# Optimization experiments

Measured on AMD Instinct MI355X. Metric: run time of the kernel, lower is better.

The kernel has to match this reference:

```python
import jax, jax.numpy as jnp
import numpy as np

N_E = 8192
E_DIM = 64
EPS = 1e-12  # torch F.normalize eps


def l2_normalize(x):
    n = jnp.linalg.norm(x, axis=-1, keepdims=True)
    return x / jnp.maximum(n, EPS)


def setup_inputs() -> dict:
    key = jax.random.key(0)
    k1, k2 = jax.random.split(key)
    z = jax.random.normal(k1, (8, E_DIM, 64, 64), dtype=jnp.float32)  # [B, C, H, W]
    # init: uniform(-1/n_e, 1/n_e) then L2-normalized (l2_norm=True)
    emb = jax.random.uniform(k2, (N_E, E_DIM), dtype=jnp.float32,
                             minval=-1.0 / N_E, maxval=1.0 / N_E)
    emb = l2_normalize(emb)
    return {"z": z, "embedding": emb}


def reference(z, embedding):
    # b c h w -> b h w c
    zt = jnp.transpose(z, (0, 2, 3, 1))
    zn = l2_normalize(zt)                      # l2_norm=True path
    z_flat = zn.reshape(-1, zn.shape[-1])      # [B*H*W, e_dim]
    e = l2_normalize(embedding)                # [n_e, e_dim]

    # squared L2 distances: ||z||^2 + ||e||^2 - 2 z e^T
    d = (jnp.sum(z_flat ** 2, axis=1, keepdims=True)
         + jnp.sum(e ** 2, axis=1)
         - 2.0 * jnp.einsum('bd,nd->bn', z_flat, e))  # [B*H*W, n_e]

    min_encoding_indices = jnp.argmin(d, axis=1)       # [B*H*W]
    z_q = e[min_encoding_indices].reshape(zn.shape)    # gather codebook

    # straight-through estimator (eval mode: commit_loss is None)
    z_q = zn + jax.lax.stop_gradient(z_q - zn)
    z_q = jnp.transpose(z_q, (0, 3, 1, 2))             # b h w c -> b c h w
    return z_q, min_encoding_indices
```

## Files before the change

kernel.cpp:

```cpp
#include <hip/hip_runtime.h>


#define NPIX 32768
#define NE   8192
#define EDIM 64
#define HW   4096
#define NSTAGE 128
#define KSPLIT 8
#define CPS  (NE / KSPLIT)
#define NSTG (CPS / NSTAGE)
#define MARGIN1 6.0e-4f
#define NSET 2

typedef _Float16 f16x8 __attribute__((ext_vector_type(8)));
typedef float f32x4  __attribute__((ext_vector_type(4)));

__device__ __forceinline__ short f2h_bits(float x) {
    _Float16 h = (_Float16)x;
    short s; __builtin_memcpy(&s, &h, 2); return s;
}
__device__ __forceinline__ unsigned int order_u32(float f) {
    unsigned int s = __float_as_uint(f);
    return (s & 0x80000000u) ? ~s : (s | 0x80000000u);
}
__device__ __forceinline__ void gload_lds16(const void* g, void* l) {
    __builtin_amdgcn_global_load_lds(
        (const __attribute__((address_space(1))) void*)g,
        (__attribute__((address_space(3))) void*)l, 16, 0, 0);
}

__global__ __launch_bounds__(256) void k_prep(const float* __restrict__ emb,
                                              const float* __restrict__ z,
                                              float* __restrict__ e_norm,
                                              float* __restrict__ se_half,
                                              short* __restrict__ esw,
                                              float* __restrict__ zn,
                                              unsigned* __restrict__ counter) {
    if (blockIdx.x == 0 && threadIdx.x == 0) counter[0] = 0u;
    if (blockIdx.x < NE / 4) {
        const int wave = threadIdx.x >> 6;
        const int lane = threadIdx.x & 63;
        const int n = blockIdx.x * 4 + wave;
        float v = emb[n * EDIM + lane];
        float ss = v * v;
        #pragma unroll
        for (int off = 32; off; off >>= 1) ss += __shfl_xor(ss, off, 64);
        const float inv = 1.0f / fmaxf(sqrtf(ss), 1e-12f);
        const float en = v * inv;
        e_norm[n * EDIM + lane] = en;
        const int grp = n >> 6, cs = n & 63;
        const int sub = cs >> 4, colb = cs & 15;
        const int o = lane >> 3, j = lane & 7;
        const int slot = ((o & 3) * 16 + colb) * 8 + j;
        esw[grp * 4096 + (sub * 2 + (o >> 2)) * 512 + slot] = f2h_bits(en);
        float s2 = en * en;
        #pragma unroll
        for (int off = 32; off; off >>= 1) s2 += __shfl_xor(s2, off, 64);
        if (lane == 0) se_half[n] = 0.5f * s2;
    } else {
        const int p = (blockIdx.x - NE / 4) * 256 + threadIdx.x;
        const int b = p >> 12, hw = p & (HW - 1);
        const float* zp = z + b * (EDIM * HW) + hw;
        float v[EDIM];
        #pragma unroll
        for (int c = 0; c < EDIM; ++c) v[c] = zp[c * HW];
        float ss = 0.0f;
        #pragma unroll
        for (int c = 0; c < EDIM; ++c) ss = fmaf(v[c], v[c], ss);
        const float inv = 1.0f / fmaxf(sqrtf(ss), 1e-12f);
        #pragma unroll
        for (int c4 = 0; c4 < 16; ++c4) {
            float4 o;
            o.x = v[c4 * 4 + 0] * inv;
            o.y = v[c4 * 4 + 1] * inv;
            o.z = v[c4 * 4 + 2] * inv;
            o.w = v[c4 * 4 + 3] * inv;
            *(float4*)(zn + p * EDIM + c4 * 4) = o;
        }
    }
}

__global__ __launch_bounds__(256, 1) void k_mfma(const float* __restrict__ zn,
                                                 const short* __restrict__ esw,
                                                 float2* __restrict__ pv,
                                                 unsigned* __restrict__ pi)
{
    __shared__ __align__(16) short es[2][NSTAGE * EDIM];

    const int tid  = threadIdx.x;
    const int wave = tid >> 6, lane = tid & 63;
    const int quad = lane >> 4, col = lane & 15;
    const int p0   = blockIdx.x * 128 + wave * 32;
    const int g    = blockIdx.y;
    const int kbase = g * CPS;

    f16x8 ah[NSET][2];
    #pragma unroll
    for (int s = 0; s < NSET; ++s) {
        const float* zr = zn + (p0 + s * 16 + col) * EDIM;
        #pragma unroll
        for (int kc = 0; kc < 2; ++kc) {
            float f[8];
            *(float4*)(f + 0) = *(const float4*)(zr + kc * 32 + quad * 8 + 0);
            *(float4*)(f + 4) = *(const float4*)(zr + kc * 32 + quad * 8 + 4);
            #pragma unroll
            for (int i = 0; i < 8; ++i) ah[s][kc][i] = (_Float16)f[i];
        }
    }

    float b1[NSET][4], b2[NSET][4];
    #pragma unroll
    for (int s = 0; s < NSET; ++s)
        #pragma unroll
        for (int r = 0; r < 4; ++r) { b1[s][r] = 0.0f; b2[s][r] = 0.0f; }

    const f32x4 cini = {2.0f, 2.0f, 2.0f, 2.0f};

    const int combo0 = wave * 4;
    const char* gsrc0 = (const char*)esw + (size_t)kbase * 128
                        + combo0 * 1024 + lane * 16;
    #pragma unroll
    for (int it = 0; it < 4; ++it)
        gload_lds16(gsrc0 + it * 1024, (char*)&es[0][0] + (combo0 + it) * 1024);

    for (int nb = 0; nb < NSTG; ++nb) {
        const int cur = nb & 1;
        __syncthreads();
        if (nb + 1 < NSTG) {
            const char* gsrc = gsrc0 + (size_t)(nb + 1) * (NSTAGE * EDIM * 2);
            #pragma unroll
            for (int it = 0; it < 4; ++it)
                gload_lds16(gsrc + it * 1024,
                            (char*)&es[cur ^ 1][0] + (combo0 + it) * 1024);
        }

        const short* esb = es[cur];
        #pragma unroll
        for (int sub = 0; sub < 8; ++sub) {
            const short* base = esb + sub * 1024;
            const f16x8 bh0 = *(const f16x8*)(base + lane * 8);
            const f16x8 bh1 = *(const f16x8*)(base + 512 + lane * 8);
            const unsigned sid = (unsigned)((nb << 3) | sub);
            #pragma unroll
            for (int s = 0; s < NSET; ++s) {
                f32x4 acc;
                acc = __builtin_amdgcn_mfma_f32_16x16x32_f16(ah[s][0], bh0, cini, 0, 0, 0);
                acc = __builtin_amdgcn_mfma_f32_16x16x32_f16(ah[s][1], bh1, acc, 0, 0, 0);
                #pragma unroll
                for (int r = 0; r < 4; ++r) {
                    const float v = __uint_as_float(
                        (__float_as_uint(acc[r]) & 0xFFFFFFC0u) | sid);
                    b2[s][r] = __builtin_amdgcn_fmed3f(v, b2[s][r], b1[s][r]);
                    b1[s][r] = fmaxf(b1[s][r], v);
                }
            }
        }
    }

    int i1[NSET][4];
    #pragma unroll
    for (int s = 0; s < NSET; ++s)
        #pragma unroll
        for (int r = 0; r < 4; ++r) {
            const unsigned id6 = __float_as_uint(b1[s][r]) & 63u;
            i1[s][r] = kbase + (int)(id6 << 4) + col;
        }

    #pragma unroll
    for (int m = 1; m <= 8; m <<= 1) {
        #pragma unroll
        for (int s = 0; s < NSET; ++s)
            #pragma unroll
            for (int r = 0; r < 4; ++r) {
                const float ob1 = __shfl_xor(b1[s][r], m, 64);
                const int   oi1 = __shfl_xor(i1[s][r], m, 64);
                const float ob2 = __shfl_xor(b2[s][r], m, 64);
                const bool take = (ob1 > b1[s][r]) || (ob1 == b1[s][r] && oi1 < i1[s][r]);
                b2[s][r] = fmaxf(fmaxf(b2[s][r], ob2), fminf(b1[s][r], ob1));
                b1[s][r] = take ? ob1 : b1[s][r];
                i1[s][r] = take ? oi1 : i1[s][r];
            }
    }
    if (col == 0) {
        #pragma unroll
        for (int s = 0; s < NSET; ++s)
            #pragma unroll
            for (int r = 0; r < 4; ++r) {
                const int p = p0 + s * 16 + quad * 4 + r;
                pv[g * NPIX + p] = make_float2(b1[s][r], b2[s][r]);
                pi[g * NPIX + p] = (unsigned)i1[s][r];
            }
    }
}

__global__ __launch_bounds__(256) void k_merge(const float2* __restrict__ pv,
                                               const unsigned* __restrict__ pi,
                                               const float* __restrict__ zn,
                                               const float* __restrict__ e_norm,
                                               const float* __restrict__ se_half,
                                               unsigned* __restrict__ idx_arr,
                                               unsigned* __restrict__ list2,
                                               unsigned* __restrict__ counter,
                                               unsigned long long* __restrict__ packed) {
    const int p = blockIdx.x * 256 + threadIdx.x;
    float2 v[KSPLIT]; unsigned ix[KSPLIT];
    #pragma unroll
    for (int gg = 0; gg < KSPLIT; ++gg) {
        v[gg] = pv[gg * NPIX + p];
        ix[gg] = pi[gg * NPIX + p];
    }
    float gb1 = v[0].x; unsigned gi1 = ix[0]; int win = 0;
    #pragma unroll
    for (int gg = 1; gg < KSPLIT; ++gg)
        if (v[gg].x > gb1) { gb1 = v[gg].x; gi1 = ix[gg]; win = gg; }
    float gb2 = -3.0e38f;
    #pragma unroll
    for (int gg = 0; gg < KSPLIT; ++gg) {
        gb2 = fmaxf(gb2, v[gg].y);
        if (gg != win) gb2 = fmaxf(gb2, v[gg].x);
    }
    const float thr = gb1 - MARGIN1;
    if (gb2 < thr) {
        idx_arr[p] = gi1;
        return;
    }
    bool esc = false;
    #pragma unroll
    for (int gg = 0; gg < KSPLIT; ++gg) esc |= (v[gg].y >= thr);
    if (esc) {
        packed[p] = ~0ull;
        idx_arr[p] = 0x80000000u | gi1;
        const unsigned pos = atomicAdd(&counter[0], 1u);
        if (pos < NPIX) list2[pos] = p;
        return;
    }
    float zr[EDIM];
    #pragma unroll
    for (int c4 = 0; c4 < 16; ++c4)
        *(float4*)(zr + c4 * 4) = *(const float4*)(zn + (size_t)p * EDIM + c4 * 4);
    float best = 3.0e38f; int bidx = 0x7FFFFFFF;
    #pragma unroll
    for (int gg = 0; gg < KSPLIT; ++gg) {
        if (v[gg].x >= thr) {
            const int c = (int)ix[gg];
            const float* er = e_norm + (size_t)c * EDIM;
            float s = 0.0f;
            #pragma unroll
            for (int k = 0; k < EDIM; ++k) s = fmaf(zr[k], er[k], s);
            const float d = se_half[c] - s;
            if (d < best || (d == best && c < bidx)) { best = d; bidx = c; }
        }
    }
    idx_arr[p] = (unsigned)bidx;
}

__global__ __launch_bounds__(256) void k_recheck(const float* __restrict__ zn,
                                                 const float* __restrict__ e_norm,
                                                 const float* __restrict__ se_half,
                                                 const unsigned* __restrict__ list2,
                                                 const unsigned* __restrict__ counter,
                                                 unsigned long long* __restrict__ packed) {
    const int lane  = threadIdx.x & 63;
    const int k     = lane >> 4;
    const int m     = lane & 15;
    const int wglob = (blockIdx.x * 256 + threadIdx.x) >> 6;
    const int nwav  = (gridDim.x * 256) >> 6;
    int cnt = (int)counter[0]; if (cnt > NPIX) cnt = NPIX;
    const int nitems = cnt * 16;
    const float4* e4 = (const float4*)e_norm;

    for (int item = wglob; item < nitems; item += nwav) {
        const int p     = (int)list2[item >> 4];
        const int chunk = item & 15;
        const float4 zv = *(const float4*)(zn + (size_t)p * EDIM + m * 4);
        float best = 3.0e38f; int bidx = 0;
        for (int t4 = 0; t4 < 32; ++t4) {
            float s[4]; int n[4];
            #pragma unroll
            for (int j = 0; j < 4; ++j) {
                n[j] = chunk * 512 + (t4 * 4 + j) * 4 + k;
                const float4 ev = e4[n[j] * 16 + m];
                s[j] = fmaf(zv.w, ev.w, fmaf(zv.z, ev.z,
                       fmaf(zv.y, ev.y, zv.x * ev.x)));
            }
            #pragma unroll
            for (int j = 0; j < 4; ++j) s[j] += __shfl_xor(s[j], 1, 64);
            #pragma unroll
            for (int j = 0; j < 4; ++j) s[j] += __shfl_xor(s[j], 2, 64);
            #pragma unroll
            for (int j = 0; j < 4; ++j) s[j] += __shfl_xor(s[j], 4, 64);
            #pragma unroll
            for (int j = 0; j < 4; ++j) s[j] += __shfl_xor(s[j], 8, 64);
            #pragma unroll
            for (int j = 0; j < 4; ++j) {
                const float d = se_half[n[j]] - s[j];
                if (d < best) { best = d; bidx = n[j]; }
            }
        }
        #pragma unroll
        for (int mm = 1; mm <= 32; mm <<= 1) {
            const float ob = __shfl_xor(best, mm, 64);
            const int   oi = __shfl_xor(bidx, mm, 64);
            if (ob < best || (ob == best && oi < bidx)) { best = ob; bidx = oi; }
        }
        if (lane == 0) {
            const unsigned long long key =
                ((unsigned long long)order_u32(best) << 32) | (unsigned)bidx;
            atomicMin(&packed[p], key);
        }
    }
}

__global__ __launch_bounds__(256) void k_finalize(const unsigned* __restrict__ idx_arr,
                                                  const unsigned long long* __restrict__ packed,
                                                  const float* __restrict__ e_norm,
                                                  float* __restrict__ out) {
    const int pl = threadIdx.x & 63;
    const int q  = threadIdx.x >> 6;
    const int p  = blockIdx.x * 64 + pl;
    const unsigned v = idx_arr[p];
    const int bidx = (v & 0x80000000u) ? (int)(packed[p] & 0xFFFFFFFFull)
                                       : (int)v;
    if (q == 0) out[NPIX * EDIM + p] = (float)bidx;
    const int b = p >> 12, hw = p & (HW - 1);
    float* op = out + b * (EDIM * HW) + hw;
    const float4* ep4 = (const float4*)(e_norm + (size_t)bidx * EDIM + q * 16);
    #pragma unroll
    for (int j = 0; j < 4; ++j) {
        const float4 e = ep4[j];
        const int c = q * 16 + j * 4;
        op[(c + 0) * HW] = e.x; op[(c + 1) * HW] = e.y;
        op[(c + 2) * HW] = e.z; op[(c + 3) * HW] = e.w;
    }
}

extern "C" void kernel_launch(void* const* d_in, const int* in_sizes, int n_in,
                              void* d_out, int out_size, void* d_ws, size_t ws_size,
                              hipStream_t stream) {
    const float* z   = (const float*)d_in[0];
    const float* emb = (const float*)d_in[1];
    float* out = (float*)d_out;

    float* e_norm  = (float*)d_ws;
    float* se_half = e_norm + NE * EDIM;
    short* esw = (short*)(se_half + NE);
    float* zn = (float*)(esw + NE * EDIM);
    unsigned* idx_arr = (unsigned*)(zn + NPIX * EDIM);
    unsigned* list2   = idx_arr + NPIX;
    unsigned* counter = list2 + NPIX;
    unsigned long long* packed = (unsigned long long*)(counter + 64);
    float2*   pv = (float2*)(packed + NPIX);
    unsigned* pi = (unsigned*)(pv + KSPLIT * NPIX);

    k_prep<<<NE / 4 + NPIX / 256, 256, 0, stream>>>(emb, z, e_norm, se_half,
                                                    esw, zn, counter);
    k_mfma<<<dim3(NPIX / 128, KSPLIT), 256, 0, stream>>>(zn, esw, pv, pi);
    k_merge<<<NPIX / 256, 256, 0, stream>>>(pv, pi, zn, e_norm, se_half,
                                            idx_arr, list2, counter, packed);
    k_recheck<<<1024, 256, 0, stream>>>(zn, e_norm, se_half, list2, counter, packed);
    k_finalize<<<NPIX / 64, 256, 0, stream>>>(idx_arr, packed, e_norm, out);
}
```

Before: 165.3 us.

## Fuse merge, recheck and finalize into one per-block post kernel

Replaces the three kernels that ran after the MFMA pass (merge, global recheck queue, finalize) with a single kernel. Each 64-pixel block merges the split partial results, keeps its own work queue of full-codebook rescans in shared memory, resolves them with shared-memory atomicMin, and writes the output. This removes two launches, the global counter and list, and the round trips through global memory. The cost is that rescans are no longer spread across the whole GPU, so blocks holding many ambiguous pixels can become stragglers. Ambiguous pixels are also now split per partition (two chunks per flagged split) rather than scanning the whole codebook.

```diff
diff --git a/kernel.cpp b/kernel.cpp
--- a/kernel.cpp
+++ b/kernel.cpp
@@ -34,9 +34,7 @@
                                               float* __restrict__ e_norm,
                                               float* __restrict__ se_half,
                                               short* __restrict__ esw,
-                                              float* __restrict__ zn,
-                                              unsigned* __restrict__ counter) {
-    if (blockIdx.x == 0 && threadIdx.x == 0) counter[0] = 0u;
+                                              float* __restrict__ zn) {
     if (blockIdx.x < NE / 4) {
         const int wave = threadIdx.x >> 6;
         const int lane = threadIdx.x & 63;
@@ -193,85 +191,89 @@
     }
 }
 
-__global__ __launch_bounds__(256) void k_merge(const float2* __restrict__ pv,
-                                               const unsigned* __restrict__ pi,
-                                               const float* __restrict__ zn,
-                                               const float* __restrict__ e_norm,
-                                               const float* __restrict__ se_half,
-                                               unsigned* __restrict__ idx_arr,
-                                               unsigned* __restrict__ list2,
-                                               unsigned* __restrict__ counter,
-                                               unsigned long long* __restrict__ packed) {
-    const int p = blockIdx.x * 256 + threadIdx.x;
-    float2 v[KSPLIT]; unsigned ix[KSPLIT];
-    #pragma unroll
-    for (int gg = 0; gg < KSPLIT; ++gg) {
-        v[gg] = pv[gg * NPIX + p];
-        ix[gg] = pi[gg * NPIX + p];
-    }
-    float gb1 = v[0].x; unsigned gi1 = ix[0]; int win = 0;
-    #pragma unroll
-    for (int gg = 1; gg < KSPLIT; ++gg)
-        if (v[gg].x > gb1) { gb1 = v[gg].x; gi1 = ix[gg]; win = gg; }
-    float gb2 = -3.0e38f;
-    #pragma unroll
-    for (int gg = 0; gg < KSPLIT; ++gg) {
-        gb2 = fmaxf(gb2, v[gg].y);
-        if (gg != win) gb2 = fmaxf(gb2, v[gg].x);
-    }
-    const float thr = gb1 - MARGIN1;
-    if (gb2 < thr) {
-        idx_arr[p] = gi1;
-        return;
-    }
-    bool esc = false;
-    #pragma unroll
-    for (int gg = 0; gg < KSPLIT; ++gg) esc |= (v[gg].y >= thr);
-    if (esc) {
-        packed[p] = ~0ull;
-        idx_arr[p] = 0x80000000u | gi1;
-        const unsigned pos = atomicAdd(&counter[0], 1u);
-        if (pos < NPIX) list2[pos] = p;
-        return;
-    }
-    float zr[EDIM];
-    #pragma unroll
-    for (int c4 = 0; c4 < 16; ++c4)
-        *(float4*)(zr + c4 * 4) = *(const float4*)(zn + (size_t)p * EDIM + c4 * 4);
-    float best = 3.0e38f; int bidx = 0x7FFFFFFF;
-    #pragma unroll
-    for (int gg = 0; gg < KSPLIT; ++gg) {
-        if (v[gg].x >= thr) {
-            const int c = (int)ix[gg];
-            const float* er = e_norm + (size_t)c * EDIM;
-            float s = 0.0f;
-            #pragma unroll
-            for (int k = 0; k < EDIM; ++k) s = fmaf(zr[k], er[k], s);
-            const float d = se_half[c] - s;
-            if (d < best || (d == best && c < bidx)) { best = d; bidx = c; }
-        }
-    }
-    idx_arr[p] = (unsigned)bidx;
-}
-
-__global__ __launch_bounds__(256) void k_recheck(const float* __restrict__ zn,
-                                                 const float* __restrict__ e_norm,
-                                                 const float* __restrict__ se_half,
-                                                 const unsigned* __restrict__ list2,
-                                                 const unsigned* __restrict__ counter,
-                                                 unsigned long long* __restrict__ packed) {
-    const int lane  = threadIdx.x & 63;
-    const int k     = lane >> 4;
-    const int m     = lane & 15;
-    const int wglob = (blockIdx.x * 256 + threadIdx.x) >> 6;
-    const int nwav  = (gridDim.x * 256) >> 6;
-    int cnt = (int)counter[0]; if (cnt > NPIX) cnt = NPIX;
-    const int nitems = cnt * 16;
+__global__ __launch_bounds__(256) void k_post(const float2* __restrict__ pv,
+                                              const unsigned* __restrict__ pi,
+                                              const float* __restrict__ zn,
+                                              const float* __restrict__ e_norm,
+                                              const float* __restrict__ se_half,
+                                              float* __restrict__ out) {
+    __shared__ unsigned s_q[1024];
+    __shared__ unsigned long long s_key[64];
+    __shared__ int s_idx[64];
+    __shared__ int s_qcnt;
+
+    const int tid  = threadIdx.x;
+    const int wave = tid >> 6, lane = tid & 63;
+    const int p0   = blockIdx.x * 64;
+
+    if (tid == 0) s_qcnt = 0;
+    __syncthreads();
+
+    if (wave == 0) {
+        const int p = p0 + lane;
+        float2 v[KSPLIT]; unsigned ix[KSPLIT];
+        #pragma unroll
+        for (int gg = 0; gg < KSPLIT; ++gg) {
+            v[gg] = pv[gg * NPIX + p];
+            ix[gg] = pi[gg * NPIX + p];
+        }
+        float gb1 = v[0].x; unsigned gi1 = ix[0]; int win = 0;
+        #pragma unroll
+        for (int gg = 1; gg < KSPLIT; ++gg)
+            if (v[gg].x > gb1) { gb1 = v[gg].x; gi1 = ix[gg]; win = gg; }
+        float gb2 = -3.0e38f;
+        #pragma unroll
+        for (int gg = 0; gg < KSPLIT; ++gg) {
+            gb2 = fmaxf(gb2, v[gg].y);
+            if (gg != win) gb2 = fmaxf(gb2, v[gg].x);
+        }
+        const float thr = gb1 - MARGIN1;
+        int idx; unsigned long long key = ~0ull; bool esc = false;
+        if (gb2 < thr) {
+            idx = (int)gi1;
+        } else {
+            float zr[EDIM];
+            #pragma unroll
+            for (int c4 = 0; c4 < 16; ++c4)
+                *(float4*)(zr + c4 * 4) =
+                    *(const float4*)(zn + (size_t)p * EDIM + c4 * 4);
+            float best = 3.0e38f; int bidx = 0x7FFFFFFF;
+            #pragma unroll
+            for (int gg = 0; gg < KSPLIT; ++gg) {
+                if (v[gg].x >= thr) {
+                    const int c = (int)ix[gg];
+                    const float* er = e_norm + (size_t)c * EDIM;
+                    float s = 0.0f;
+                    #pragma unroll
+                    for (int k = 0; k < EDIM; ++k) s = fmaf(zr[k], er[k], s);
+                    const float d = se_half[c] - s;
+                    if (d < best || (d == best && c < bidx)) { best = d; bidx = c; }
+                }
+            }
+            idx = bidx;
+            key = ((unsigned long long)order_u32(best) << 32) | (unsigned)bidx;
+            #pragma unroll
+            for (int gg = 0; gg < KSPLIT; ++gg) {
+                if (v[gg].y >= thr) {
+                    esc = true;
+                    const int base = atomicAdd(&s_qcnt, 2);
+                    s_q[base]     = (unsigned)lane | ((unsigned)(gg * 2)     << 6);
+                    s_q[base + 1] = (unsigned)lane | ((unsigned)(gg * 2 + 1) << 6);
+                }
+            }
+        }
+        s_key[lane] = key;
+        s_idx[lane] = esc ? -1 : idx;
+    }
+    __syncthreads();
+
+    const int qn = s_qcnt;
+    const int k = lane >> 4, m = lane & 15;
     const float4* e4 = (const float4*)e_norm;
-
-    for (int item = wglob; item < nitems; item += nwav) {
-        const int p     = (int)list2[item >> 4];
-        const int chunk = item & 15;
+    for (int e = wave; e < qn; e += 4) {
+        const unsigned ent = s_q[e];
+        const int pl = (int)(ent & 63u), chunk = (int)(ent >> 6);
+        const int p = p0 + pl;
         const float4 zv = *(const float4*)(zn + (size_t)p * EDIM + m * 4);
         float best = 3.0e38f; int bidx = 0;
         for (int t4 = 0; t4 < 32; ++t4) {
@@ -304,33 +306,29 @@
             if (ob < best || (ob == best && oi < bidx)) { best = ob; bidx = oi; }
         }
         if (lane == 0) {
-            const unsigned long long key =
+            const unsigned long long kk =
                 ((unsigned long long)order_u32(best) << 32) | (unsigned)bidx;
-            atomicMin(&packed[p], key);
-        }
-    }
-}
-
-__global__ __launch_bounds__(256) void k_finalize(const unsigned* __restrict__ idx_arr,
-                                                  const unsigned long long* __restrict__ packed,
-                                                  const float* __restrict__ e_norm,
-                                                  float* __restrict__ out) {
-    const int pl = threadIdx.x & 63;
-    const int q  = threadIdx.x >> 6;
-    const int p  = blockIdx.x * 64 + pl;
-    const unsigned v = idx_arr[p];
-    const int bidx = (v & 0x80000000u) ? (int)(packed[p] & 0xFFFFFFFFull)
-                                       : (int)v;
+            atomicMin(&s_key[pl], kk);
+        }
+    }
+    __syncthreads();
+    if (wave == 0 && s_idx[lane] < 0)
+        s_idx[lane] = (int)(s_key[lane] & 0xFFFFFFFFull);
+    __syncthreads();
+
+    const int p = p0 + lane;
+    const int bidx = s_idx[lane];
+    const int q = wave;
     if (q == 0) out[NPIX * EDIM + p] = (float)bidx;
     const int b = p >> 12, hw = p & (HW - 1);
     float* op = out + b * (EDIM * HW) + hw;
     const float4* ep4 = (const float4*)(e_norm + (size_t)bidx * EDIM + q * 16);
     #pragma unroll
     for (int j = 0; j < 4; ++j) {
-        const float4 e = ep4[j];
+        const float4 ev = ep4[j];
         const int c = q * 16 + j * 4;
-        op[(c + 0) * HW] = e.x; op[(c + 1) * HW] = e.y;
-        op[(c + 2) * HW] = e.z; op[(c + 3) * HW] = e.w;
+        op[(c + 0) * HW] = ev.x; op[(c + 1) * HW] = ev.y;
+        op[(c + 2) * HW] = ev.z; op[(c + 3) * HW] = ev.w;
     }
 }
 
@@ -345,18 +343,11 @@
     float* se_half = e_norm + NE * EDIM;
     short* esw = (short*)(se_half + NE);
     float* zn = (float*)(esw + NE * EDIM);
-    unsigned* idx_arr = (unsigned*)(zn + NPIX * EDIM);
-    unsigned* list2   = idx_arr + NPIX;
-    unsigned* counter = list2 + NPIX;
-    unsigned long long* packed = (unsigned long long*)(counter + 64);
-    float2*   pv = (float2*)(packed + NPIX);
+    float2*   pv = (float2*)(zn + NPIX * EDIM);
     unsigned* pi = (unsigned*)(pv + KSPLIT * NPIX);
 
     k_prep<<<NE / 4 + NPIX / 256, 256, 0, stream>>>(emb, z, e_norm, se_half,
-                                                    esw, zn, counter);
+                                                    esw, zn);
     k_mfma<<<dim3(NPIX / 128, KSPLIT), 256, 0, stream>>>(zn, esw, pv, pi);
-    k_merge<<<NPIX / 256, 256, 0, stream>>>(pv, pi, zn, e_norm, se_half,
-                                            idx_arr, list2, counter, packed);
-    k_recheck<<<1024, 256, 0, stream>>>(zn, e_norm, se_half, list2, counter, packed);
-    k_finalize<<<NPIX / 64, 256, 0, stream>>>(idx_arr, packed, e_norm, out);
-}
+    k_post<<<NPIX / 64, 256, 0, stream>>>(pv, pi, zn, e_norm, se_half, out);
+}
```

Result: slower. 175.4 us (+6.1%).

## Fuse finalize into merge/recheck and rescan only flagged codebook splits

Applied to the files above, without the earlier changes.

The merge kernel now writes the gathered codebook row and index straight to the output for resolved pixels, which removes the separate finalize kernel and its idx/packed buffers. Ambiguous pixels are queued with a bitmask of the splits whose second-best value was close, together with the exact best key found so far. The recheck kernel gives each pixel one wavefront, scans only the flagged 1024-entry splits instead of all 8192 entries, and writes the output itself. This removes a launch and most of the recheck work, but moves the strided output writes into merge and loads a single wavefront with a serial per-pixel loop.

```diff
diff --git a/kernel.cpp b/kernel.cpp
--- a/kernel.cpp
+++ b/kernel.cpp
@@ -193,16 +193,16 @@
     }
 }
 
-__global__ __launch_bounds__(256) void k_merge(const float2* __restrict__ pv,
+__global__ __launch_bounds__(128) void k_merge(const float2* __restrict__ pv,
                                                const unsigned* __restrict__ pi,
                                                const float* __restrict__ zn,
                                                const float* __restrict__ e_norm,
                                                const float* __restrict__ se_half,
-                                               unsigned* __restrict__ idx_arr,
-                                               unsigned* __restrict__ list2,
+                                               unsigned* __restrict__ list,
+                                               unsigned long long* __restrict__ lkey,
                                                unsigned* __restrict__ counter,
-                                               unsigned long long* __restrict__ packed) {
-    const int p = blockIdx.x * 256 + threadIdx.x;
+                                               float* __restrict__ out) {
+    const int p = blockIdx.x * 128 + threadIdx.x;
     float2 v[KSPLIT]; unsigned ix[KSPLIT];
     #pragma unroll
     for (int gg = 0; gg < KSPLIT; ++gg) {
@@ -220,117 +220,117 @@
         if (gg != win) gb2 = fmaxf(gb2, v[gg].x);
     }
     const float thr = gb1 - MARGIN1;
+    int bidx;
     if (gb2 < thr) {
-        idx_arr[p] = gi1;
-        return;
-    }
-    bool esc = false;
-    #pragma unroll
-    for (int gg = 0; gg < KSPLIT; ++gg) esc |= (v[gg].y >= thr);
-    if (esc) {
-        packed[p] = ~0ull;
-        idx_arr[p] = 0x80000000u | gi1;
-        const unsigned pos = atomicAdd(&counter[0], 1u);
-        if (pos < NPIX) list2[pos] = p;
-        return;
-    }
-    float zr[EDIM];
-    #pragma unroll
-    for (int c4 = 0; c4 < 16; ++c4)
-        *(float4*)(zr + c4 * 4) = *(const float4*)(zn + (size_t)p * EDIM + c4 * 4);
-    float best = 3.0e38f; int bidx = 0x7FFFFFFF;
-    #pragma unroll
-    for (int gg = 0; gg < KSPLIT; ++gg) {
-        if (v[gg].x >= thr) {
-            const int c = (int)ix[gg];
-            const float* er = e_norm + (size_t)c * EDIM;
-            float s = 0.0f;
-            #pragma unroll
-            for (int k = 0; k < EDIM; ++k) s = fmaf(zr[k], er[k], s);
-            const float d = se_half[c] - s;
-            if (d < best || (d == best && c < bidx)) { best = d; bidx = c; }
-        }
-    }
-    idx_arr[p] = (unsigned)bidx;
+        bidx = (int)gi1;
+    } else {
+        float zr[EDIM];
+        #pragma unroll
+        for (int c4 = 0; c4 < 16; ++c4)
+            *(float4*)(zr + c4 * 4) =
+                *(const float4*)(zn + (size_t)p * EDIM + c4 * 4);
+        float best = 3.0e38f; bidx = 0x7FFFFFFF;
+        #pragma unroll
+        for (int gg = 0; gg < KSPLIT; ++gg) {
+            if (v[gg].x >= thr) {
+                const int c = (int)ix[gg];
+                const float* er = e_norm + (size_t)c * EDIM;
+                float s = 0.0f;
+                #pragma unroll
+                for (int k = 0; k < EDIM; ++k) s = fmaf(zr[k], er[k], s);
+                const float d = se_half[c] - s;
+                if (d < best || (d == best && c < bidx)) { best = d; bidx = c; }
+            }
+        }
+        unsigned mask = 0;
+        #pragma unroll
+        for (int gg = 0; gg < KSPLIT; ++gg)
+            if (v[gg].y >= thr) mask |= (1u << gg);
+        if (mask) {
+            const unsigned pos = atomicAdd(&counter[0], 1u);
+            list[pos] = (unsigned)p | (mask << 16);
+            lkey[pos] = ((unsigned long long)order_u32(best) << 32) | (unsigned)bidx;
+            return;
+        }
+    }
+    out[NPIX * EDIM + p] = (float)bidx;
+    const int b = p >> 12, hw = p & (HW - 1);
+    float* op = out + b * (EDIM * HW) + hw;
+    const float4* ep4 = (const float4*)(e_norm + (size_t)bidx * EDIM);
+    #pragma unroll
+    for (int j = 0; j < 16; ++j) {
+        const float4 e = ep4[j];
+        const int c = j * 4;
+        op[(c + 0) * HW] = e.x; op[(c + 1) * HW] = e.y;
+        op[(c + 2) * HW] = e.z; op[(c + 3) * HW] = e.w;
+    }
 }
 
 __global__ __launch_bounds__(256) void k_recheck(const float* __restrict__ zn,
                                                  const float* __restrict__ e_norm,
                                                  const float* __restrict__ se_half,
-                                                 const unsigned* __restrict__ list2,
+                                                 const unsigned* __restrict__ list,
+                                                 const unsigned long long* __restrict__ lkey,
                                                  const unsigned* __restrict__ counter,
-                                                 unsigned long long* __restrict__ packed) {
+                                                 float* __restrict__ out) {
     const int lane  = threadIdx.x & 63;
     const int k     = lane >> 4;
     const int m     = lane & 15;
     const int wglob = (blockIdx.x * 256 + threadIdx.x) >> 6;
     const int nwav  = (gridDim.x * 256) >> 6;
     int cnt = (int)counter[0]; if (cnt > NPIX) cnt = NPIX;
-    const int nitems = cnt * 16;
     const float4* e4 = (const float4*)e_norm;
 
-    for (int item = wglob; item < nitems; item += nwav) {
-        const int p     = (int)list2[item >> 4];
-        const int chunk = item & 15;
+    for (int item = wglob; item < cnt; item += nwav) {
+        const unsigned e = list[item];
+        const int p = (int)(e & 0xFFFFu);
+        const unsigned mask = e >> 16;
+        unsigned long long key = lkey[item];
         const float4 zv = *(const float4*)(zn + (size_t)p * EDIM + m * 4);
-        float best = 3.0e38f; int bidx = 0;
-        for (int t4 = 0; t4 < 32; ++t4) {
-            float s[4]; int n[4];
-            #pragma unroll
-            for (int j = 0; j < 4; ++j) {
-                n[j] = chunk * 512 + (t4 * 4 + j) * 4 + k;
-                const float4 ev = e4[n[j] * 16 + m];
-                s[j] = fmaf(zv.w, ev.w, fmaf(zv.z, ev.z,
-                       fmaf(zv.y, ev.y, zv.x * ev.x)));
-            }
-            #pragma unroll
-            for (int j = 0; j < 4; ++j) s[j] += __shfl_xor(s[j], 1, 64);
-            #pragma unroll
-            for (int j = 0; j < 4; ++j) s[j] += __shfl_xor(s[j], 2, 64);
-            #pragma unroll
-            for (int j = 0; j < 4; ++j) s[j] += __shfl_xor(s[j], 4, 64);
-            #pragma unroll
-            for (int j = 0; j < 4; ++j) s[j] += __shfl_xor(s[j], 8, 64);
-            #pragma unroll
-            for (int j = 0; j < 4; ++j) {
-                const float d = se_half[n[j]] - s[j];
-                if (d < best) { best = d; bidx = n[j]; }
-            }
-        }
-        #pragma unroll
-        for (int mm = 1; mm <= 32; mm <<= 1) {
-            const float ob = __shfl_xor(best, mm, 64);
-            const int   oi = __shfl_xor(bidx, mm, 64);
-            if (ob < best || (ob == best && oi < bidx)) { best = ob; bidx = oi; }
-        }
-        if (lane == 0) {
-            const unsigned long long key =
-                ((unsigned long long)order_u32(best) << 32) | (unsigned)bidx;
-            atomicMin(&packed[p], key);
-        }
-    }
-}
-
-__global__ __launch_bounds__(256) void k_finalize(const unsigned* __restrict__ idx_arr,
-                                                  const unsigned long long* __restrict__ packed,
-                                                  const float* __restrict__ e_norm,
-                                                  float* __restrict__ out) {
-    const int pl = threadIdx.x & 63;
-    const int q  = threadIdx.x >> 6;
-    const int p  = blockIdx.x * 64 + pl;
-    const unsigned v = idx_arr[p];
-    const int bidx = (v & 0x80000000u) ? (int)(packed[p] & 0xFFFFFFFFull)
-                                       : (int)v;
-    if (q == 0) out[NPIX * EDIM + p] = (float)bidx;
-    const int b = p >> 12, hw = p & (HW - 1);
-    float* op = out + b * (EDIM * HW) + hw;
-    const float4* ep4 = (const float4*)(e_norm + (size_t)bidx * EDIM + q * 16);
-    #pragma unroll
-    for (int j = 0; j < 4; ++j) {
-        const float4 e = ep4[j];
-        const int c = q * 16 + j * 4;
-        op[(c + 0) * HW] = e.x; op[(c + 1) * HW] = e.y;
-        op[(c + 2) * HW] = e.z; op[(c + 3) * HW] = e.w;
+        for (int g = 0; g < KSPLIT; ++g) {
+            if (!(mask & (1u << g))) continue;
+            #pragma unroll
+            for (int half = 0; half < 2; ++half) {
+                const int chunk = g * 2 + half;
+                float best = 3.0e38f; int bidx = 0;
+                for (int t4 = 0; t4 < 32; ++t4) {
+                    float s[4]; int n[4];
+                    #pragma unroll
+                    for (int j = 0; j < 4; ++j) {
+                        n[j] = chunk * 512 + (t4 * 4 + j) * 4 + k;
+                        const float4 ev = e4[n[j] * 16 + m];
+                        s[j] = fmaf(zv.w, ev.w, fmaf(zv.z, ev.z,
+                               fmaf(zv.y, ev.y, zv.x * ev.x)));
+                    }
+                    #pragma unroll
+                    for (int j = 0; j < 4; ++j) s[j] += __shfl_xor(s[j], 1, 64);
+                    #pragma unroll
+                    for (int j = 0; j < 4; ++j) s[j] += __shfl_xor(s[j], 2, 64);
+                    #pragma unroll
+                    for (int j = 0; j < 4; ++j) s[j] += __shfl_xor(s[j], 4, 64);
+                    #pragma unroll
+                    for (int j = 0; j < 4; ++j) s[j] += __shfl_xor(s[j], 8, 64);
+                    #pragma unroll
+                    for (int j = 0; j < 4; ++j) {
+                        const float d = se_half[n[j]] - s[j];
+                        if (d < best) { best = d; bidx = n[j]; }
+                    }
+                }
+                #pragma unroll
+                for (int mm = 1; mm <= 32; mm <<= 1) {
+                    const float ob = __shfl_xor(best, mm, 64);
+                    const int   oi = __shfl_xor(bidx, mm, 64);
+                    if (ob < best || (ob == best && oi < bidx)) { best = ob; bidx = oi; }
+                }
+                const unsigned long long kk =
+                    ((unsigned long long)order_u32(best) << 32) | (unsigned)bidx;
+                key = (kk < key) ? kk : key;
+            }
+        }
+        const int bidx = (int)(key & 0xFFFFFFFFull);
+        if (lane == 0) out[NPIX * EDIM + p] = (float)bidx;
+        const int b = p >> 12, hw = p & (HW - 1);
+        out[b * (EDIM * HW) + lane * HW + hw] = e_norm[(size_t)bidx * EDIM + lane];
     }
 }
 
@@ -345,18 +345,17 @@
     float* se_half = e_norm + NE * EDIM;
     short* esw = (short*)(se_half + NE);
     float* zn = (float*)(esw + NE * EDIM);
-    unsigned* idx_arr = (unsigned*)(zn + NPIX * EDIM);
-    unsigned* list2   = idx_arr + NPIX;
-    unsigned* counter = list2 + NPIX;
-    unsigned long long* packed = (unsigned long long*)(counter + 64);
-    float2*   pv = (float2*)(packed + NPIX);
+    unsigned* list    = (unsigned*)(zn + NPIX * EDIM);
+    unsigned* counter = list + NPIX;
+    unsigned long long* lkey = (unsigned long long*)(counter + 64);
+    float2*   pv = (float2*)(lkey + NPIX);
     unsigned* pi = (unsigned*)(pv + KSPLIT * NPIX);
 
     k_prep<<<NE / 4 + NPIX / 256, 256, 0, stream>>>(emb, z, e_norm, se_half,
                                                     esw, zn, counter);
     k_mfma<<<dim3(NPIX / 128, KSPLIT), 256, 0, stream>>>(zn, esw, pv, pi);
-    k_merge<<<NPIX / 256, 256, 0, stream>>>(pv, pi, zn, e_norm, se_half,
-                                            idx_arr, list2, counter, packed);
-    k_recheck<<<1024, 256, 0, stream>>>(zn, e_norm, se_half, list2, counter, packed);
-    k_finalize<<<NPIX / 64, 256, 0, stream>>>(idx_arr, packed, e_norm, out);
-}
+    k_merge<<<NPIX / 128, 128, 0, stream>>>(pv, pi, zn, e_norm, se_half,
+                                            list, lkey, counter, out);
+    k_recheck<<<256, 256, 0, stream>>>(zn, e_norm, se_half, list, lkey,
+                                       counter, out);
+}
```

Measured after the change: 180.2 us. 1.09x slower.
